# Kernel tuning notes

Measured on AMD Instinct MI355X. Metric: run time of the kernel, lower is better.

## Reference

```python
import jax, jax.numpy as jnp
import numpy as np

N_NODES = 100000
N_EDGES = 1600000
C_IN = 32
C_OUT = 32


def setup_inputs() -> dict:
    key = jax.random.key(0)
    ks = jax.random.split(key, 12)
    x = jax.random.normal(ks[0], (N_NODES, C_IN), dtype=jnp.float32)
    edge_index = jax.random.randint(ks[1], (2, N_EDGES), 0, N_NODES, dtype=jnp.int64)
    def glorot(k, fan_in, fan_out):
        s = jnp.sqrt(6.0 / (fan_in + fan_out))
        return jax.random.uniform(k, (fan_in, fan_out), jnp.float32, -s, s)
    return {
        "x": x,
        "edge_index": edge_index,
        "W1": glorot(ks[2], C_IN, C_OUT),  "b1": jnp.zeros((C_OUT,), jnp.float32),
        "W2": glorot(ks[3], C_OUT, C_OUT), "b2": jnp.zeros((C_OUT,), jnp.float32),
        "Wmu": glorot(ks[4], C_OUT, C_OUT), "bmu": jnp.zeros((C_OUT,), jnp.float32),
        "Wlv": glorot(ks[5], C_OUT, C_OUT), "blv": jnp.zeros((C_OUT,), jnp.float32),
    }


def _gcn_norm(edge_index, n_nodes):
    # PyG GCNConv default: add self-loops, symmetric normalization.
    loops = jnp.arange(n_nodes, dtype=edge_index.dtype)
    src = jnp.concatenate([edge_index[0], loops])
    dst = jnp.concatenate([edge_index[1], loops])
    deg = jax.ops.segment_sum(jnp.ones_like(dst, dtype=jnp.float32), dst,
                              num_segments=n_nodes)
    dis = jnp.where(deg > 0, jax.lax.rsqrt(deg), 0.0)  # deg^-1/2
    norm = dis[src] * dis[dst]  # [E + N]
    return src, dst, norm


def _gcn_layer(x, src, dst, norm, W, b, n_nodes):
    h = x @ W                                   # [N, Cout]
    msg = h[src] * norm[:, None]                # gather + scale, [E+N, Cout]
    out = jax.ops.segment_sum(msg, dst, num_segments=n_nodes)  # scatter-add
    return out + b


def reference(x, edge_index, W1, b1, W2, b2, Wmu, bmu, Wlv, blv):
    n = x.shape[0]
    src, dst, norm = _gcn_norm(edge_index, n)
    h = jax.nn.relu(_gcn_layer(x, src, dst, norm, W1, b1, n))
    h = jax.nn.relu(_gcn_layer(h, src, dst, norm, W2, b2, n))
    mu = _gcn_layer(h, src, dst, norm, Wmu, bmu, n)
    logvar = _gcn_layer(h, src, dst, norm, Wlv, blv, n)
    return (mu, logvar)
```

## Files before the change

### kernel.cpp

```cpp
#include <hip/hip_runtime.h>
#include <hip/hip_fp16.h>


#define BK_BITS 9
#define BK      (1 << BK_BITS)
#define BMASK   (BK - 1)
#define EPT     16
#define CHUNK   (256 * EPT)
#define CAP     16384

typedef int   vint4   __attribute__((ext_vector_type(4)));
typedef uint  vuint4  __attribute__((ext_vector_type(4)));
typedef float vfloat4 __attribute__((ext_vector_type(4)));

#define NTL(p) __builtin_nontemporal_load(p)

__global__ void k_bucket(const int* __restrict__ src, const int* __restrict__ dst,
                         int* __restrict__ bcur, int* __restrict__ ebuf, int E) {
    __shared__ int lcnt[256];
    __shared__ int lbase[256];
    int t = threadIdx.x;
    lcnt[t] = 0;
    __syncthreads();
    int e0 = blockIdx.x * CHUNK;
    int pk[EPT];
#pragma unroll
    for (int i = 0; i < EPT; ++i) {
        int e = e0 + i * 256 + t;
        pk[i] = -1;
        if (e < E) {
            int d = NTL(dst + e);
            int b = d >> BK_BITS;
            int off = atomicAdd(&lcnt[b], 1);
            pk[i] = (b << 21) | (off << BK_BITS) | (d & BMASK);
        }
    }
    __syncthreads();
    lbase[t] = t * CAP + atomicAdd(&bcur[t], lcnt[t]);
    __syncthreads();
#pragma unroll
    for (int i = 0; i < EPT; ++i) {
        int e = e0 + i * 256 + t;
        if (e < E) {
            int b   = pk[i] >> 21;
            int off = (pk[i] >> BK_BITS) & 4095;
            int dl  = pk[i] & BMASK;
            int pos = lbase[b] + off;
            if (pos < (b + 1) * CAP)
                ebuf[pos] = (NTL(src + e) << BK_BITS) | dl;
        }
    }
}

__global__ void k_finalize(const int* __restrict__ bcur, int* __restrict__ starts,
                           float* __restrict__ dis, const int* __restrict__ ebuf,
                           int* __restrict__ es, const float* __restrict__ x,
                           __half* __restrict__ g0, int n, int E) {
    __shared__ int   hist[BK];
    __shared__ int   sc[BK];
    __shared__ int   sb[256];
    __shared__ float disL[BK];
    int b = blockIdx.x, t = threadIdx.x;
    if (t < 256) sb[t] = min(bcur[t], CAP);
    hist[t] = 0;
    __syncthreads();
    for (int o = 1; o < 256; o <<= 1) {
        int xv = 0;
        if (t < 256 && t >= o) xv = sb[t - o];
        __syncthreads();
        if (t < 256) sb[t] += xv;
        __syncthreads();
    }
    int cnt = min(bcur[b], CAP);
    int beg = sb[b] - cnt;
    const int* eb = ebuf + (size_t)b * CAP;
    for (int j = t; j < cnt; j += BK)
        atomicAdd(&hist[eb[j] & BMASK], 1);
    __syncthreads();
    int cv = hist[t];
    sc[t] = cv;
    __syncthreads();
    for (int o = 1; o < BK; o <<= 1) {
        int xv = (t >= o) ? sc[t - o] : 0;
        __syncthreads();
        sc[t] += xv;
        __syncthreads();
    }
    int excl = sc[t] - cv;
    int gnode = (b << BK_BITS) + t;
    float dv = rsqrtf((float)cv + 1.0f);
    disL[t] = dv;
    if (gnode < n) {
        starts[gnode] = beg + excl;
        dis[gnode] = dv;
    }
    if (b == 0 && t == 0) starts[n] = E;
    hist[t] = excl;
    __syncthreads();
    for (int j = t; j < cnt; j += BK) {
        int v = eb[j];
        int off = atomicAdd(&hist[v & BMASK], 1);
        es[beg + off] = v >> BK_BITS;
    }
    int node0 = b << BK_BITS;
    const float4* x4 = (const float4*)x;
    uint2* g2 = (uint2*)g0;
    for (int idx = t; idx < BK * 8; idx += BK) {
        int r = idx >> 3, lane = idx & 7;
        int nd = node0 + r;
        if (nd < n) {
            float d = disL[r];
            float4 v = x4[(size_t)nd * 8 + lane];
            __half2 lo = __floats2half2_rn(d * v.x, d * v.y);
            __half2 hi = __floats2half2_rn(d * v.z, d * v.w);
            uint2 u;
            u.x = *(unsigned int*)&lo;
            u.y = *(unsigned int*)&hi;
            g2[(size_t)nd * 8 + lane] = u;
        }
    }
}

__device__ inline void acc8(uint4 u, float* s) {
    __half2 h0 = *(__half2*)&u.x, h1 = *(__half2*)&u.y;
    __half2 h2 = *(__half2*)&u.z, h3 = *(__half2*)&u.w;
    float2 f0 = __half22float2(h0), f1 = __half22float2(h1);
    float2 f2 = __half22float2(h2), f3 = __half22float2(h3);
    s[0] += f0.x; s[1] += f0.y; s[2] += f1.x; s[3] += f1.y;
    s[4] += f2.x; s[5] += f2.y; s[6] += f3.x; s[7] += f3.y;
}

template <bool OUT16>
__global__ void k_agg(const int* __restrict__ starts, const int* __restrict__ es,
                      const float* __restrict__ dis, const __half* __restrict__ g,
                      void* __restrict__ outp, int n) {
    int t = threadIdx.x;
    int node = blockIdx.x * 64 + (t >> 2);
    if (node >= n) return;
    int lane = t & 3;
    const uint4* g4 = (const uint4*)g;
    float s[8] = {0, 0, 0, 0, 0, 0, 0, 0};
    acc8(g4[(size_t)node * 4 + lane], s);
    int j = starts[node], end = starts[node + 1];
    while (j < end && (j & 3)) {
        acc8(g4[(size_t)es[j] * 4 + lane], s);
        ++j;
    }
    for (; j + 8 <= end; j += 8) {
        int4 e0 = *(const int4*)(es + j);
        int4 e1 = *(const int4*)(es + j + 4);
        uint4 u0 = g4[(size_t)e0.x * 4 + lane];
        uint4 u1 = g4[(size_t)e0.y * 4 + lane];
        uint4 u2 = g4[(size_t)e0.z * 4 + lane];
        uint4 u3 = g4[(size_t)e0.w * 4 + lane];
        uint4 u4 = g4[(size_t)e1.x * 4 + lane];
        uint4 u5 = g4[(size_t)e1.y * 4 + lane];
        uint4 u6 = g4[(size_t)e1.z * 4 + lane];
        uint4 u7 = g4[(size_t)e1.w * 4 + lane];
        acc8(u0, s); acc8(u1, s); acc8(u2, s); acc8(u3, s);
        acc8(u4, s); acc8(u5, s); acc8(u6, s); acc8(u7, s);
    }
    if (j + 4 <= end) {
        int4 e0 = *(const int4*)(es + j);
        uint4 u0 = g4[(size_t)e0.x * 4 + lane];
        uint4 u1 = g4[(size_t)e0.y * 4 + lane];
        uint4 u2 = g4[(size_t)e0.z * 4 + lane];
        uint4 u3 = g4[(size_t)e0.w * 4 + lane];
        acc8(u0, s); acc8(u1, s); acc8(u2, s); acc8(u3, s);
        j += 4;
    }
    for (; j < end; ++j) acc8(g4[(size_t)es[j] * 4 + lane], s);
    float dd = dis[node];
    if (OUT16) {
        __half2 h0 = __floats2half2_rn(dd * s[0], dd * s[1]);
        __half2 h1 = __floats2half2_rn(dd * s[2], dd * s[3]);
        __half2 h2 = __floats2half2_rn(dd * s[4], dd * s[5]);
        __half2 h3 = __floats2half2_rn(dd * s[6], dd * s[7]);
        uint4 u;
        u.x = *(unsigned int*)&h0; u.y = *(unsigned int*)&h1;
        u.z = *(unsigned int*)&h2; u.w = *(unsigned int*)&h3;
        ((uint4*)outp)[(size_t)node * 4 + lane] = u;
    } else {
        float4 o0 = make_float4(dd * s[0], dd * s[1], dd * s[2], dd * s[3]);
        float4 o1 = make_float4(dd * s[4], dd * s[5], dd * s[6], dd * s[7]);
        float4* op = (float4*)outp + (size_t)node * 8 + lane * 2;
        op[0] = o0;
        op[1] = o1;
    }
}


__global__ void k_gemm32(const __half* __restrict__ in, const float* __restrict__ W,
                         const float* __restrict__ bias, const float* __restrict__ dis,
                         __half* __restrict__ gout, int n, int ntiles) {
    __shared__ float Ws[32][33];
    __shared__ float Xs[32][33];
    int t = threadIdx.x;
    for (int i = t; i < 1024; i += 256) Ws[i >> 5][i & 31] = W[i];
    int c = t & 31;
    int rbase = t >> 5;
    float bc = bias[c];
    for (int tile = blockIdx.x; tile < ntiles; tile += gridDim.x) {
        int node0 = tile * 32;
        __syncthreads();
        if (t < 128) {
            int r = t >> 2, seg = t & 3;
            int node = node0 + r;
            float f[8] = {0, 0, 0, 0, 0, 0, 0, 0};
            if (node < n) {
                vuint4 u = NTL((const vuint4*)in + (size_t)node * 4 + seg);
                unsigned int w[4] = {u.x, u.y, u.z, u.w};
#pragma unroll
                for (int i = 0; i < 4; ++i) {
                    float2 ff = __half22float2(*(__half2*)&w[i]);
                    f[2 * i] = ff.x; f[2 * i + 1] = ff.y;
                }
            }
#pragma unroll
            for (int i = 0; i < 8; ++i) Xs[r][seg * 8 + i] = f[i];
        }
        __syncthreads();
#pragma unroll
        for (int rr = 0; rr < 4; ++rr) {
            int r = rbase + rr * 8;
            int node = node0 + r;
            if (node >= n) continue;
            float sum = bc;
#pragma unroll
            for (int k = 0; k < 32; ++k) sum += Xs[r][k] * Ws[k][c];
            gout[(size_t)node * 32 + c] = __float2half_rn(dis[node] * fmaxf(sum, 0.f));
        }
    }
}

__global__ void k_gemm64(const float* __restrict__ in, const float* __restrict__ Wmu,
                         const float* __restrict__ Wlv, const float* __restrict__ bmu,
                         const float* __restrict__ blv, float* __restrict__ out,
                         int n, int ntiles) {
    __shared__ float Ws[32][64];
    __shared__ float Xs[16][33];
    int t = threadIdx.x;
    for (int i = t; i < 1024; i += 256) {
        int k = i >> 5, cc = i & 31;
        Ws[k][cc]      = Wmu[i];
        Ws[k][cc + 32] = Wlv[i];
    }
    int c = t & 63;
    int rbase = t >> 6;
    float bc = (c < 32) ? bmu[c] : blv[c - 32];
    for (int tile = blockIdx.x; tile < ntiles; tile += gridDim.x) {
        int node0 = tile * 16;
        __syncthreads();
        if (t < 128) {
            int r = t >> 3, seg = t & 7;
            int node = node0 + r;
            vfloat4 v = {0.f, 0.f, 0.f, 0.f};
            if (node < n) v = NTL((const vfloat4*)in + (size_t)node * 8 + seg);
            Xs[r][seg * 4]     = v.x;
            Xs[r][seg * 4 + 1] = v.y;
            Xs[r][seg * 4 + 2] = v.z;
            Xs[r][seg * 4 + 3] = v.w;
        }
        __syncthreads();
#pragma unroll
        for (int rr = 0; rr < 4; ++rr) {
            int r = rbase + rr * 4;
            int node = node0 + r;
            if (node >= n) continue;
            float sum = bc;
#pragma unroll
            for (int k = 0; k < 32; ++k) sum += Xs[r][k] * Ws[k][c];
            if (c < 32) out[(size_t)node * 32 + c] = sum;
            else        out[(size_t)n * 32 + (size_t)node * 32 + (c - 32)] = sum;
        }
    }
}


extern "C" void kernel_launch(void* const* d_in, const int* in_sizes, int n_in,
                              void* d_out, int out_size, void* d_ws, size_t ws_size,
                              hipStream_t stream) {
    const float* x   = (const float*)d_in[0];
    const int*   ei  = (const int*)d_in[1];
    const float* W1  = (const float*)d_in[2];
    const float* b1  = (const float*)d_in[3];
    const float* W2  = (const float*)d_in[4];
    const float* b2  = (const float*)d_in[5];
    const float* Wmu = (const float*)d_in[6];
    const float* bmu = (const float*)d_in[7];
    const float* Wlv = (const float*)d_in[8];
    const float* blv = (const float*)d_in[9];
    float* out = (float*)d_out;

    int n = in_sizes[0] / 32;
    int E = in_sizes[1] / 2;
    const int* src = ei;
    const int* dst = ei + E;
    int nbuck = (n + BK - 1) >> BK_BITS;

    int*    bcur   = (int*)d_ws;
    int     npad   = (n + 4) & ~3;
    int*    starts = bcur + 256;
    float*  dis    = (float*)(starts + npad);
    int*    es     = (int*)(dis + n);
    float*  a32    = (float*)(es + E);
    __half* aH     = (__half*)(a32 + (size_t)n * 32);
    __half* gA     = aH + (size_t)n * 32;
    __half* gB     = gA + (size_t)n * 32;
    int*    ebuf   = (int*)(gB + (size_t)n * 32);

    int nblk = (E + CHUNK - 1) / CHUNK;
    int agrid = (n + 63) / 64;
    int t32 = (n + 31) / 32;
    int t64 = (n + 15) / 16;

    hipMemsetAsync(bcur, 0, 256 * sizeof(int), stream);
    k_bucket<<<nblk, 256, 0, stream>>>(src, dst, bcur, ebuf, E);
    k_finalize<<<nbuck, BK, 0, stream>>>(bcur, starts, dis, ebuf, es, x, gA, n, E);

    k_agg<true><<<agrid, 256, 0, stream>>>(starts, es, dis, gA, aH, n);
    k_gemm32<<<1280, 256, 0, stream>>>(aH, W1, b1, dis, gB, n, t32);

    k_agg<true><<<agrid, 256, 0, stream>>>(starts, es, dis, gB, aH, n);
    k_gemm32<<<1280, 256, 0, stream>>>(aH, W2, b2, dis, gA, n, t32);

    k_agg<false><<<agrid, 256, 0, stream>>>(starts, es, dis, gA, a32, n);
    k_gemm64<<<1280, 256, 0, stream>>>(a32, Wmu, Wlv, bmu, blv, out, n, t64);
}
```

Before: 294.1 us.

## Fuse neighbor aggregation with the following dense transform in each GCN layer

Each layer's gather-aggregate kernel is merged with the 32x32 (or dual 32x64) matrix multiply that follows it. The aggregated row is staged in shared memory and multiplied there, so the intermediate aH/a32 buffers and their global write and re-read go away, along with three kernel launches. The cost is extra shared memory and registers per block, which may lower occupancy for the latency-bound gather phase.

```diff
diff --git a/kernel.cpp b/kernel.cpp
--- a/kernel.cpp
+++ b/kernel.cpp
@@ -130,16 +130,10 @@
     s[4] += f2.x; s[5] += f2.y; s[6] += f3.x; s[7] += f3.y;
 }
 
-template <bool OUT16>
-__global__ void k_agg(const int* __restrict__ starts, const int* __restrict__ es,
-                      const float* __restrict__ dis, const __half* __restrict__ g,
-                      void* __restrict__ outp, int n) {
-    int t = threadIdx.x;
-    int node = blockIdx.x * 64 + (t >> 2);
-    if (node >= n) return;
-    int lane = t & 3;
-    const uint4* g4 = (const uint4*)g;
-    float s[8] = {0, 0, 0, 0, 0, 0, 0, 0};
+__device__ inline void gather32(const int* __restrict__ starts,
+                                const int* __restrict__ es,
+                                const uint4* __restrict__ g4,
+                                int node, int lane, float* s) {
     acc8(g4[(size_t)node * 4 + lane], s);
     int j = starts[node], end = starts[node + 1];
     while (j < end && (j & 3)) {
@@ -170,109 +164,95 @@
         j += 4;
     }
     for (; j < end; ++j) acc8(g4[(size_t)es[j] * 4 + lane], s);
-    float dd = dis[node];
-    if (OUT16) {
-        __half2 h0 = __floats2half2_rn(dd * s[0], dd * s[1]);
-        __half2 h1 = __floats2half2_rn(dd * s[2], dd * s[3]);
-        __half2 h2 = __floats2half2_rn(dd * s[4], dd * s[5]);
-        __half2 h3 = __floats2half2_rn(dd * s[6], dd * s[7]);
+}
+
+__global__ __launch_bounds__(256)
+void k_fused16(const int* __restrict__ starts, const int* __restrict__ es,
+               const float* __restrict__ dis, const __half* __restrict__ g,
+               const float* __restrict__ W, const float* __restrict__ bias,
+               __half* __restrict__ gout, int n) {
+    __shared__ float Ws[32][33];
+    __shared__ float Xs[64][33];
+    int t = threadIdx.x;
+    for (int i = t; i < 1024; i += 256) Ws[i >> 5][i & 31] = W[i];
+    int r = t >> 2, lane = t & 3;
+    int node = blockIdx.x * 64 + r;
+    bool alive = node < n;
+    float dd = 0.f;
+    if (alive) {
+        float s[8] = {0, 0, 0, 0, 0, 0, 0, 0};
+        gather32(starts, es, (const uint4*)g, node, lane, s);
+        dd = dis[node];
+#pragma unroll
+        for (int i = 0; i < 8; ++i) Xs[r][lane * 8 + i] = dd * s[i];
+    }
+    __syncthreads();
+    if (alive) {
+        int c0 = lane * 8;
+        float acc[8];
+#pragma unroll
+        for (int i = 0; i < 8; ++i) acc[i] = bias[c0 + i];
+#pragma unroll 8
+        for (int k = 0; k < 32; ++k) {
+            float xv = Xs[r][k];
+#pragma unroll
+            for (int i = 0; i < 8; ++i) acc[i] += xv * Ws[k][c0 + i];
+        }
+        __half2 h0 = __floats2half2_rn(dd * fmaxf(acc[0], 0.f), dd * fmaxf(acc[1], 0.f));
+        __half2 h1 = __floats2half2_rn(dd * fmaxf(acc[2], 0.f), dd * fmaxf(acc[3], 0.f));
+        __half2 h2 = __floats2half2_rn(dd * fmaxf(acc[4], 0.f), dd * fmaxf(acc[5], 0.f));
+        __half2 h3 = __floats2half2_rn(dd * fmaxf(acc[6], 0.f), dd * fmaxf(acc[7], 0.f));
         uint4 u;
         u.x = *(unsigned int*)&h0; u.y = *(unsigned int*)&h1;
         u.z = *(unsigned int*)&h2; u.w = *(unsigned int*)&h3;
-        ((uint4*)outp)[(size_t)node * 4 + lane] = u;
-    } else {
-        float4 o0 = make_float4(dd * s[0], dd * s[1], dd * s[2], dd * s[3]);
-        float4 o1 = make_float4(dd * s[4], dd * s[5], dd * s[6], dd * s[7]);
-        float4* op = (float4*)outp + (size_t)node * 8 + lane * 2;
-        op[0] = o0;
-        op[1] = o1;
-    }
-}
-
-
-__global__ void k_gemm32(const __half* __restrict__ in, const float* __restrict__ W,
-                         const float* __restrict__ bias, const float* __restrict__ dis,
-                         __half* __restrict__ gout, int n, int ntiles) {
-    __shared__ float Ws[32][33];
-    __shared__ float Xs[32][33];
-    int t = threadIdx.x;
-    for (int i = t; i < 1024; i += 256) Ws[i >> 5][i & 31] = W[i];
-    int c = t & 31;
-    int rbase = t >> 5;
-    float bc = bias[c];
-    for (int tile = blockIdx.x; tile < ntiles; tile += gridDim.x) {
-        int node0 = tile * 32;
-        __syncthreads();
-        if (t < 128) {
-            int r = t >> 2, seg = t & 3;
-            int node = node0 + r;
-            float f[8] = {0, 0, 0, 0, 0, 0, 0, 0};
-            if (node < n) {
-                vuint4 u = NTL((const vuint4*)in + (size_t)node * 4 + seg);
-                unsigned int w[4] = {u.x, u.y, u.z, u.w};
-#pragma unroll
-                for (int i = 0; i < 4; ++i) {
-                    float2 ff = __half22float2(*(__half2*)&w[i]);
-                    f[2 * i] = ff.x; f[2 * i + 1] = ff.y;
-                }
-            }
-#pragma unroll
-            for (int i = 0; i < 8; ++i) Xs[r][seg * 8 + i] = f[i];
-        }
-        __syncthreads();
-#pragma unroll
-        for (int rr = 0; rr < 4; ++rr) {
-            int r = rbase + rr * 8;
-            int node = node0 + r;
-            if (node >= n) continue;
-            float sum = bc;
-#pragma unroll
-            for (int k = 0; k < 32; ++k) sum += Xs[r][k] * Ws[k][c];
-            gout[(size_t)node * 32 + c] = __float2half_rn(dis[node] * fmaxf(sum, 0.f));
-        }
-    }
-}
-
-__global__ void k_gemm64(const float* __restrict__ in, const float* __restrict__ Wmu,
-                         const float* __restrict__ Wlv, const float* __restrict__ bmu,
-                         const float* __restrict__ blv, float* __restrict__ out,
-                         int n, int ntiles) {
-    __shared__ float Ws[32][64];
-    __shared__ float Xs[16][33];
+        ((uint4*)gout)[(size_t)node * 4 + lane] = u;
+    }
+}
+
+__global__ __launch_bounds__(256)
+void k_fused_final(const int* __restrict__ starts, const int* __restrict__ es,
+                   const float* __restrict__ dis, const __half* __restrict__ g,
+                   const float* __restrict__ Wmu, const float* __restrict__ Wlv,
+                   const float* __restrict__ bmu, const float* __restrict__ blv,
+                   float* __restrict__ out, int n) {
+    __shared__ float Ws[32][66];
+    __shared__ float Xs[64][33];
     int t = threadIdx.x;
     for (int i = t; i < 1024; i += 256) {
-        int k = i >> 5, cc = i & 31;
-        Ws[k][cc]      = Wmu[i];
-        Ws[k][cc + 32] = Wlv[i];
-    }
-    int c = t & 63;
-    int rbase = t >> 6;
-    float bc = (c < 32) ? bmu[c] : blv[c - 32];
-    for (int tile = blockIdx.x; tile < ntiles; tile += gridDim.x) {
-        int node0 = tile * 16;
-        __syncthreads();
-        if (t < 128) {
-            int r = t >> 3, seg = t & 7;
-            int node = node0 + r;
-            vfloat4 v = {0.f, 0.f, 0.f, 0.f};
-            if (node < n) v = NTL((const vfloat4*)in + (size_t)node * 8 + seg);
-            Xs[r][seg * 4]     = v.x;
-            Xs[r][seg * 4 + 1] = v.y;
-            Xs[r][seg * 4 + 2] = v.z;
-            Xs[r][seg * 4 + 3] = v.w;
-        }
-        __syncthreads();
-#pragma unroll
-        for (int rr = 0; rr < 4; ++rr) {
-            int r = rbase + rr * 4;
-            int node = node0 + r;
-            if (node >= n) continue;
-            float sum = bc;
-#pragma unroll
-            for (int k = 0; k < 32; ++k) sum += Xs[r][k] * Ws[k][c];
-            if (c < 32) out[(size_t)node * 32 + c] = sum;
-            else        out[(size_t)n * 32 + (size_t)node * 32 + (c - 32)] = sum;
-        }
+        Ws[i >> 5][i & 31]        = Wmu[i];
+        Ws[i >> 5][32 + (i & 31)] = Wlv[i];
+    }
+    int r = t >> 2, lane = t & 3;
+    int node = blockIdx.x * 64 + r;
+    bool alive = node < n;
+    if (alive) {
+        float s[8] = {0, 0, 0, 0, 0, 0, 0, 0};
+        gather32(starts, es, (const uint4*)g, node, lane, s);
+        float dd = dis[node];
+#pragma unroll
+        for (int i = 0; i < 8; ++i) Xs[r][lane * 8 + i] = dd * s[i];
+    }
+    __syncthreads();
+    if (alive) {
+        int c0 = lane * 8;
+        float am[8], al[8];
+#pragma unroll
+        for (int i = 0; i < 8; ++i) { am[i] = bmu[c0 + i]; al[i] = blv[c0 + i]; }
+#pragma unroll 4
+        for (int k = 0; k < 32; ++k) {
+            float xv = Xs[r][k];
+#pragma unroll
+            for (int i = 0; i < 8; ++i) {
+                am[i] += xv * Ws[k][c0 + i];
+                al[i] += xv * Ws[k][32 + c0 + i];
+            }
+        }
+        float4* om = (float4*)out + (size_t)node * 8 + lane * 2;
+        om[0] = make_float4(am[0], am[1], am[2], am[3]);
+        om[1] = make_float4(am[4], am[5], am[6], am[7]);
+        float4* ol = (float4*)(out + (size_t)n * 32) + (size_t)node * 8 + lane * 2;
+        ol[0] = make_float4(al[0], al[1], al[2], al[3]);
+        ol[1] = make_float4(al[4], al[5], al[6], al[7]);
     }
 }
 
@@ -303,27 +283,18 @@
     int*    starts = bcur + 256;
     float*  dis    = (float*)(starts + npad);
     int*    es     = (int*)(dis + n);
-    float*  a32    = (float*)(es + E);
-    __half* aH     = (__half*)(a32 + (size_t)n * 32);
-    __half* gA     = aH + (size_t)n * 32;
+    __half* gA     = (__half*)(es + E);
     __half* gB     = gA + (size_t)n * 32;
     int*    ebuf   = (int*)(gB + (size_t)n * 32);
 
-    int nblk = (E + CHUNK - 1) / CHUNK;
+    int nblk  = (E + CHUNK - 1) / CHUNK;
     int agrid = (n + 63) / 64;
-    int t32 = (n + 31) / 32;
-    int t64 = (n + 15) / 16;
 
     hipMemsetAsync(bcur, 0, 256 * sizeof(int), stream);
     k_bucket<<<nblk, 256, 0, stream>>>(src, dst, bcur, ebuf, E);
     k_finalize<<<nbuck, BK, 0, stream>>>(bcur, starts, dis, ebuf, es, x, gA, n, E);
 
-    k_agg<true><<<agrid, 256, 0, stream>>>(starts, es, dis, gA, aH, n);
-    k_gemm32<<<1280, 256, 0, stream>>>(aH, W1, b1, dis, gB, n, t32);
-
-    k_agg<true><<<agrid, 256, 0, stream>>>(starts, es, dis, gB, aH, n);
-    k_gemm32<<<1280, 256, 0, stream>>>(aH, W2, b2, dis, gA, n, t32);
-
-    k_agg<false><<<agrid, 256, 0, stream>>>(starts, es, dis, gA, a32, n);
-    k_gemm64<<<1280, 256, 0, stream>>>(a32, Wmu, Wlv, bmu, blv, out, n, t64);
-}
+    k_fused16<<<agrid, 256, 0, stream>>>(starts, es, dis, gA, W1, b1, gB, n);
+    k_fused16<<<agrid, 256, 0, stream>>>(starts, es, dis, gB, W2, b2, gA, n);
+    k_fused_final<<<agrid, 256, 0, stream>>>(starts, es, dis, gA, Wmu, Wlv, bmu, blv, out, n);
+}
```

Result: faster. 249.2 us (-15.3%).
